# Optimization experiments

Hardware: AMD Instinct MI355X
Metric: run time of the kernel (lower is better)

The kernel has to match this reference:

```python
import jax, jax.numpy as jnp
import numpy as np

Q = 9          # D2Q9
G = 8          # dihedral group of the square
X = YD = 768   # spatial grid
HID = 32       # tau_net hidden width
N_IN = 6       # moments with order <= 2 (indices 0..5, contiguous by construction)
LOWER_TAU = 0.8


def _build_stencil():
    # D2Q9 velocities and weights
    e = np.array([[0, 0], [1, 0], [0, 1], [-1, 0], [0, -1],
                  [1, 1], [-1, 1], [-1, -1], [1, -1]], dtype=np.float64)
    w = np.array([4 / 9] + [1 / 9] * 4 + [1 / 36] * 4, dtype=np.float64)
    # natural moment matrix: rows are monomials ex^px * ey^py, ordered so that
    # moment_order = [0,1,1,2,2,2,3,3,4]  ->  in_indices=[0..5], out_indices=[6,7,8]
    exps = [(0, 0), (1, 0), (0, 1), (2, 0), (1, 1), (0, 2), (2, 1), (1, 2), (2, 2)]
    M = np.stack([e[:, 0] ** px * e[:, 1] ** py for px, py in exps])  # [Q, Q]
    Minv = np.linalg.inv(M)
    # symmetry group of the square: 4 rotations x {id, x-axis reflection}
    rots = [np.array([[np.cos(a), -np.sin(a)], [np.sin(a), np.cos(a)]])
            for a in (0.0, np.pi / 2, np.pi, 3 * np.pi / 2)]
    refl = np.array([[1.0, 0.0], [0.0, -1.0]])
    Rs = rots + [r @ refl for r in rots]
    perms = []
    for R in Rs:
        Re = np.rint(e @ R.T)
        P = np.zeros((Q, Q))
        for i in range(Q):
            j = int(np.where((e == Re[i]).all(axis=1))[0][0])
            P[j, i] = 1.0  # velocity i maps to velocity j under R
        perms.append(P)
    P = np.stack(perms)                                   # [G, Q, Q]
    actions = np.einsum('qp,gpr,rs->gqs', M, P, Minv)      # moment action  M P M^-1
    Pt = P.transpose(0, 2, 1)                              # P^-1 = P^T
    inv_actions = np.einsum('qp,gpr,rs->gqs', M, Pt, Minv)
    return (M.astype(np.float32), Minv.astype(np.float32),
            actions.astype(np.float32), inv_actions.astype(np.float32),
            e.astype(np.float32), w.astype(np.float32))


def setup_inputs() -> dict:
    key = jax.random.key(0)
    kf, k1, k2, k3 = jax.random.split(key, 4)
    M, Minv, actions, inv_actions, e, w = _build_stencil()
    f = jax.random.uniform(kf, (Q, X, YD), dtype=jnp.float32)
    s = 0.1
    return {
        'f': f,
        'M': jnp.asarray(M), 'Minv': jnp.asarray(Minv),
        'actions': jnp.asarray(actions), 'inv_actions': jnp.asarray(inv_actions),
        'e': jnp.asarray(e), 'w': jnp.asarray(w),
        'W1': jax.random.normal(k1, (N_IN, HID), jnp.float32) * s,
        'b1': jnp.zeros((HID,), jnp.float32),
        'W2': jax.random.normal(k2, (HID, HID), jnp.float32) * s,
        'b2': jnp.zeros((HID,), jnp.float32),
        'W3': jax.random.normal(k3, (HID, Q - N_IN), jnp.float32) * s,
        'b3': jnp.zeros((Q - N_IN,), jnp.float32),
    }


def reference(f, M, Minv, actions, inv_actions, e, w, W1, b1, W2, b2, W3, b3):
    # --- moment transform: m = M f, moved to channel-last [X, Y, Q] ---
    m = jnp.einsum('qp,pxy->xyq', M, f)
    # --- equivariant tau net on low-order moments ---
    x_in = m[..., :N_IN]                                   # in_indices = 0..5
    Ainv = inv_actions[:, :N_IN, :N_IN]                    # [G, 6, 6]
    A = actions[:, N_IN:, N_IN:]                           # [G, 3, 3] (out_indices)
    xg = jnp.einsum('gij,xyj->gxyi', Ainv, x_in)           # [G, X, Y, 6]
    h = jax.nn.relu(xg @ W1 + b1)
    h = jax.nn.relu(h @ W2 + b2)
    o = h @ W3 + b3                                        # [G, X, Y, 3]
    out = jnp.einsum('gij,gxyj->xyi', A, o)                # sum over group -> [X, Y, 3]
    tau_hi = 1.5 + jax.nn.elu(out)                         # gt_half: > 0.5
    taus = jnp.full(m.shape, LOWER_TAU, m.dtype).at[..., N_IN:].set(tau_hi)
    # --- equilibrium moments: meq = M feq(rho, u) (quadratic BGK, cs^2=1/3) ---
    rho = m[..., 0:1]                                      # natural moments: m0=rho
    u = m[..., 1:3] / rho                                  # m1,m2 = momentum
    eu = jnp.einsum('qd,xyd->xyq', e, u)
    usq = jnp.sum(u * u, axis=-1, keepdims=True)
    feq = w * rho * (1.0 + 3.0 * eu + 4.5 * eu * eu - 1.5 * usq)
    meq = jnp.einsum('qp,xyp->xyq', M, feq)
    # --- MRT collision + inverse transform ---
    m_post = m - (m - meq) / taus
    return jnp.einsum('pq,xyq->pxy', Minv, m_post)
```

## Files before the change

### kernel.cpp

```cpp
#include <hip/hip_runtime.h>
#include <hip/hip_bf16.h>
#include <math.h>

#define Q 9
#define NPIX (768 * 768)

typedef short bf16x8 __attribute__((ext_vector_type(8)));
typedef float f32x4 __attribute__((ext_vector_type(4)));
typedef int i32x4 __attribute__((ext_vector_type(4)));

#define A1BV 512
#define A3V  1024
#define A2V  1536
#define B3TF 6656

__device__ __forceinline__ unsigned short f2bf(float x) {
    unsigned u = __builtin_bit_cast(unsigned, x);
    unsigned r = u + 0x7FFFu + ((u >> 16) & 1u);
    return (unsigned short)(r >> 16);
}

__device__ __forceinline__ unsigned pk2(float e, float o) {
    __hip_bfloat162 h = __float22bfloat162_rn(make_float2(e, o));
    unsigned u;
    __builtin_memcpy(&u, &h, 4);
    return u;
}

__device__ __forceinline__ bf16x8 mk8(unsigned w0, unsigned w1, unsigned w2, unsigned w3) {
    i32x4 t = {(int)w0, (int)w1, (int)w2, (int)w3};
    return __builtin_bit_cast(bf16x8, t);
}

__global__ void prep_kernel(const float* __restrict__ actions,
                            const float* __restrict__ inv_actions,
                            const float* __restrict__ W1,
                            const float* __restrict__ b1,
                            const float* __restrict__ W2,
                            const float* __restrict__ W3,
                            const float* __restrict__ b3,
                            short* __restrict__ wsb,
                            float* __restrict__ wsf) {
    const int idx = blockIdx.x * 256 + threadIdx.x;
    if (idx < 8192) {
        int j = idx & 7, l = (idx >> 3) & 63, g = (idx >> 9) & 7, half = idx >> 12;
        int m = l & 15, quad = l >> 4, k = quad * 8 + j;
        int feat = 8 * (m >> 2) + (m & 3) + 4 * half;
        float v = 0.f;
        if (k < 6) {
            #pragma unroll
            for (int i = 0; i < 6; i++)
                v += inv_actions[g * 81 + i * 9 + k] * W1[i * 32 + feat];
        } else if (k == 6) v = b1[feat];
        wsb[idx] = (short)f2bf(v);
    } else if (idx < 12288) {
        int t = idx - 8192;
        int j = t & 7, l = (t >> 3) & 63, g = t >> 9;
        int m = l & 15, quad = l >> 4, k = quad * 8 + j;
        float v = 0.f;
        if (m < 3) {
            #pragma unroll
            for (int j3 = 0; j3 < 3; j3++)
                v += W3[k * 3 + j3] * actions[g * 81 + (6 + m) * 9 + (6 + j3)];
        }
        wsb[idx] = (short)f2bf(v);
    } else if (idx < 13312) {
        int t = idx - 12288;
        int j = t & 7, l = (t >> 3) & 63, half = t >> 9;
        int m = l & 15, quad = l >> 4, k = quad * 8 + j;
        int feat = 8 * (m >> 2) + (m & 3) + 4 * half;
        wsb[idx] = (short)f2bf(W2[k * 32 + feat]);
    } else if (idx < 13315) {
        int t = idx - 13312;
        float acc = 0.f;
        for (int g = 0; g < 8; g++)
            #pragma unroll
            for (int j = 0; j < 3; j++)
                acc += actions[g * 81 + (6 + t) * 9 + (6 + j)] * b3[j];
        wsf[B3TF + t] = acc;
    }
}

__global__ __launch_bounds__(256, 4) void lbm_kernel(
    const float* __restrict__ f,
    const float* __restrict__ Minv,
    const float* __restrict__ w,
    const float* __restrict__ b2,
    const short* __restrict__ wsb,
    const float* __restrict__ wsf,
    float* __restrict__ out) {
    __shared__ float oL[4][64][4];

    const int tid = threadIdx.x;
    const int wv = tid >> 6;
    const int l = tid & 63;
    const int quad = l >> 4;
    const int lc = l & 15;
    const int p = blockIdx.x * 256 + tid;

    float fv0 = f[0 * NPIX + p], fv1 = f[1 * NPIX + p], fv2 = f[2 * NPIX + p];
    float fv3 = f[3 * NPIX + p], fv4 = f[4 * NPIX + p], fv5 = f[5 * NPIX + p];
    float fv6 = f[6 * NPIX + p], fv7 = f[7 * NPIX + p], fv8 = f[8 * NPIX + p];
    float sa = fv5 + fv6, sb = fv7 + fv8, sc = fv5 - fv6, sd = fv7 - fv8;
    float sab = sa + sb;
    float m8 = sab, m6 = sa - sb, m4 = sc + sd, m7 = sc - sd;
    float p13 = fv1 + fv3, d13 = fv1 - fv3, p24 = fv2 + fv4, d24 = fv2 - fv4;
    float m0 = fv0 + p13 + p24 + sab;
    float m1 = d13 + m7;
    float m2 = d24 + m6;
    float m3 = p13 + sab;
    float m5 = p24 + sab;

    unsigned mp0 = pk2(m0, m1), mp1 = pk2(m2, m3), mp2 = pk2(m4, m5);
    const unsigned CONE = 0x00003F80u;
    bf16x8 B1[4];
    #pragma unroll
    for (int nb = 0; nb < 4; nb++) {
        int src = ((nb << 4) | lc) << 2;
        unsigned a = (unsigned)__builtin_amdgcn_ds_bpermute(src, (int)mp0);
        unsigned b = (unsigned)__builtin_amdgcn_ds_bpermute(src, (int)mp1);
        unsigned c = (unsigned)__builtin_amdgcn_ds_bpermute(src, (int)mp2);
        B1[nb] = mk8(a, b, c, CONE);
    }

    const bf16x8* wsv = (const bf16x8*)wsb;
    bf16x8 a2a = wsv[A2V + l], a2b = wsv[A2V + 64 + l];
    f32x4 c2iA = *(const f32x4*)(b2 + 8 * quad);
    f32x4 c2iB = *(const f32x4*)(b2 + 8 * quad + 4);
    float b30 = wsf[B3TF + 0], b31 = wsf[B3TF + 1], b32 = wsf[B3TF + 2];
    f32x4 oinit;
    oinit[0] = (quad == 0) ? b30 : 0.f;
    oinit[1] = (quad == 0) ? b31 : 0.f;
    oinit[2] = (quad == 0) ? b32 : 0.f;
    oinit[3] = 0.f;
    f32x4 oacc[4] = {oinit, oinit, oinit, oinit};

    bf16x8 a1a = wsv[l], a1b = wsv[A1BV + l], a3 = wsv[A3V + l];

    #pragma unroll 1
    for (int g = 0; g < 8; g++) {
        const int gn = (g + 1) & 7;
        bf16x8 na1a = wsv[gn * 64 + l];
        bf16x8 na1b = wsv[A1BV + gn * 64 + l];
        bf16x8 na3  = wsv[A3V + gn * 64 + l];
        #pragma unroll
        for (int nb = 0; nb < 4; nb++) {
            f32x4 z = {0.f, 0.f, 0.f, 0.f};
            f32x4 c1a = __builtin_amdgcn_mfma_f32_16x16x32_bf16(a1a, B1[nb], z, 0, 0, 0);
            f32x4 c1b = __builtin_amdgcn_mfma_f32_16x16x32_bf16(a1b, B1[nb], z, 0, 0, 0);
            bf16x8 B2 = mk8(
                pk2(fmaxf(c1a[0], 0.f), fmaxf(c1a[1], 0.f)),
                pk2(fmaxf(c1a[2], 0.f), fmaxf(c1a[3], 0.f)),
                pk2(fmaxf(c1b[0], 0.f), fmaxf(c1b[1], 0.f)),
                pk2(fmaxf(c1b[2], 0.f), fmaxf(c1b[3], 0.f)));
            f32x4 c2a = __builtin_amdgcn_mfma_f32_16x16x32_bf16(a2a, B2, c2iA, 0, 0, 0);
            f32x4 c2b = __builtin_amdgcn_mfma_f32_16x16x32_bf16(a2b, B2, c2iB, 0, 0, 0);
            bf16x8 B3 = mk8(
                pk2(fmaxf(c2a[0], 0.f), fmaxf(c2a[1], 0.f)),
                pk2(fmaxf(c2a[2], 0.f), fmaxf(c2a[3], 0.f)),
                pk2(fmaxf(c2b[0], 0.f), fmaxf(c2b[1], 0.f)),
                pk2(fmaxf(c2b[2], 0.f), fmaxf(c2b[3], 0.f)));
            oacc[nb] = __builtin_amdgcn_mfma_f32_16x16x32_bf16(a3, B3, oacc[nb], 0, 0, 0);
        }
        a1a = na1a; a1b = na1b; a3 = na3;
    }

    if (quad == 0) {
        #pragma unroll
        for (int nb = 0; nb < 4; nb++)
            *(f32x4*)&oL[wv][nb * 16 + lc][0] = oacc[nb];
    }
    f32x4 ov = *(const f32x4*)&oL[wv][l][0];
    float o_[3] = {ov[0], ov[1], ov[2]};

    float tinv[3];
    #pragma unroll
    for (int i = 0; i < 3; i++) {
        float o = o_[i];
        float el = (o > 0.f) ? o : (__expf(o) - 1.f);
        tinv[i] = __builtin_amdgcn_rcpf(1.5f + el);
    }

    float rho = m0;
    float ir = __builtin_amdgcn_rcpf(rho);
    float ux = m1 * ir, uy = m2 * ir;
    float usq = ux * ux + uy * uy;
    float base = 1.f - 1.5f * usq;
    float w0r = w[0] * rho, w1r = w[1] * rho, w5r = w[5] * rho;
    float feq0 = w0r * base;
    float ax = 4.5f * ux * ux + base, bx = 3.f * ux;
    float feq1 = w1r * (ax + bx), feq3 = w1r * (ax - bx);
    float ay = 4.5f * uy * uy + base, by = 3.f * uy;
    float feq2 = w1r * (ay + by), feq4 = w1r * (ay - by);
    float ss = ux + uy, as_ = 4.5f * ss * ss + base, bs = 3.f * ss;
    float feq5 = w5r * (as_ + bs), feq7 = w5r * (as_ - bs);
    float dd = uy - ux, ad = 4.5f * dd * dd + base, bd = 3.f * dd;
    float feq6 = w5r * (ad + bd), feq8 = w5r * (ad - bd);

    float ea = feq5 + feq6, eb = feq7 + feq8, ec = feq5 - feq6, ed = feq7 - feq8;
    float eab = ea + eb;
    float q8 = eab, q6 = ea - eb, q4 = ec + ed, q7 = ec - ed;
    float ep13 = feq1 + feq3, ed13 = feq1 - feq3, ep24 = feq2 + feq4, ed24 = feq2 - feq4;
    float q0 = feq0 + ep13 + ep24 + eab;
    float q1 = ed13 + q7, q2 = ed24 + q6, q3 = ep13 + eab, q5 = ep24 + eab;

    float mp_[9];
    mp_[0] = m0 - (m0 - q0) * 1.25f;
    mp_[1] = m1 - (m1 - q1) * 1.25f;
    mp_[2] = m2 - (m2 - q2) * 1.25f;
    mp_[3] = m3 - (m3 - q3) * 1.25f;
    mp_[4] = m4 - (m4 - q4) * 1.25f;
    mp_[5] = m5 - (m5 - q5) * 1.25f;
    mp_[6] = m6 - (m6 - q6) * tinv[0];
    mp_[7] = m7 - (m7 - q7) * tinv[1];
    mp_[8] = m8 - (m8 - q8) * tinv[2];

    #pragma unroll
    for (int q = 0; q < 9; q++) {
        float acc = Minv[q * 9 + 0] * mp_[0];
        #pragma unroll
        for (int pp = 1; pp < 9; pp++) acc = fmaf(Minv[q * 9 + pp], mp_[pp], acc);
        __builtin_nontemporal_store(acc, &out[q * NPIX + p]);
    }
}

extern "C" void kernel_launch(void* const* d_in, const int* in_sizes, int n_in,
                              void* d_out, int out_size, void* d_ws, size_t ws_size,
                              hipStream_t stream) {
    const float* f           = (const float*)d_in[0];
    const float* Minv        = (const float*)d_in[2];
    const float* actions     = (const float*)d_in[3];
    const float* inv_actions = (const float*)d_in[4];
    const float* w           = (const float*)d_in[6];
    const float* W1          = (const float*)d_in[7];
    const float* b1          = (const float*)d_in[8];
    const float* W2          = (const float*)d_in[9];
    const float* b2          = (const float*)d_in[10];
    const float* W3          = (const float*)d_in[11];
    const float* b3          = (const float*)d_in[12];
    float* outp = (float*)d_out;
    short* wsb = (short*)d_ws;
    float* wsf = (float*)d_ws;

    prep_kernel<<<53, 256, 0, stream>>>(actions, inv_actions, W1, b1, W2, W3, b3, wsb, wsf);
    lbm_kernel<<<NPIX / 256, 256, 0, stream>>>(f, Minv, w, b2, wsb, wsf, outp);
}
```

Before: 135.3 us.

## Rewrite collision epilogue in closed form and reload f to cut register pressure

```diff
diff --git a/kernel.cpp b/kernel.cpp
--- a/kernel.cpp
+++ b/kernel.cpp
@@ -6,6 +6,7 @@
 #define NPIX (768 * 768)
 
 typedef short bf16x8 __attribute__((ext_vector_type(8)));
+typedef short s16x2 __attribute__((ext_vector_type(2)));
 typedef float f32x4 __attribute__((ext_vector_type(4)));
 typedef int i32x4 __attribute__((ext_vector_type(4)));
 
@@ -25,6 +26,13 @@
     unsigned u;
     __builtin_memcpy(&u, &h, 4);
     return u;
+}
+
+__device__ __forceinline__ unsigned relu2(unsigned d) {
+    s16x2 v = __builtin_bit_cast(s16x2, d);
+    const s16x2 z = {0, 0};
+    v = __builtin_elementwise_max(v, z);
+    return __builtin_bit_cast(unsigned, v);
 }
 
 __device__ __forceinline__ bf16x8 mk8(unsigned w0, unsigned w1, unsigned w2, unsigned w3) {
@@ -90,6 +98,8 @@
     const float* __restrict__ wsf,
     float* __restrict__ out) {
     __shared__ float oL[4][64][4];
+    (void)Minv;
+    (void)w;
 
     const int tid = threadIdx.x;
     const int wv = tid >> 6;
@@ -103,11 +113,11 @@
     float fv6 = f[6 * NPIX + p], fv7 = f[7 * NPIX + p], fv8 = f[8 * NPIX + p];
     float sa = fv5 + fv6, sb = fv7 + fv8, sc = fv5 - fv6, sd = fv7 - fv8;
     float sab = sa + sb;
-    float m8 = sab, m6 = sa - sb, m4 = sc + sd, m7 = sc - sd;
+    float m4 = sc + sd;
     float p13 = fv1 + fv3, d13 = fv1 - fv3, p24 = fv2 + fv4, d24 = fv2 - fv4;
     float m0 = fv0 + p13 + p24 + sab;
-    float m1 = d13 + m7;
-    float m2 = d24 + m6;
+    float m1 = d13 + (sc - sd);
+    float m2 = d24 + (sa - sb);
     float m3 = p13 + sab;
     float m5 = p24 + sab;
 
@@ -149,17 +159,17 @@
             f32x4 c1a = __builtin_amdgcn_mfma_f32_16x16x32_bf16(a1a, B1[nb], z, 0, 0, 0);
             f32x4 c1b = __builtin_amdgcn_mfma_f32_16x16x32_bf16(a1b, B1[nb], z, 0, 0, 0);
             bf16x8 B2 = mk8(
-                pk2(fmaxf(c1a[0], 0.f), fmaxf(c1a[1], 0.f)),
-                pk2(fmaxf(c1a[2], 0.f), fmaxf(c1a[3], 0.f)),
-                pk2(fmaxf(c1b[0], 0.f), fmaxf(c1b[1], 0.f)),
-                pk2(fmaxf(c1b[2], 0.f), fmaxf(c1b[3], 0.f)));
+                relu2(pk2(c1a[0], c1a[1])),
+                relu2(pk2(c1a[2], c1a[3])),
+                relu2(pk2(c1b[0], c1b[1])),
+                relu2(pk2(c1b[2], c1b[3])));
             f32x4 c2a = __builtin_amdgcn_mfma_f32_16x16x32_bf16(a2a, B2, c2iA, 0, 0, 0);
             f32x4 c2b = __builtin_amdgcn_mfma_f32_16x16x32_bf16(a2b, B2, c2iB, 0, 0, 0);
             bf16x8 B3 = mk8(
-                pk2(fmaxf(c2a[0], 0.f), fmaxf(c2a[1], 0.f)),
-                pk2(fmaxf(c2a[2], 0.f), fmaxf(c2a[3], 0.f)),
-                pk2(fmaxf(c2b[0], 0.f), fmaxf(c2b[1], 0.f)),
-                pk2(fmaxf(c2b[2], 0.f), fmaxf(c2b[3], 0.f)));
+                relu2(pk2(c2a[0], c2a[1])),
+                relu2(pk2(c2a[2], c2a[3])),
+                relu2(pk2(c2b[0], c2b[1])),
+                relu2(pk2(c2b[2], c2b[3])));
             oacc[nb] = __builtin_amdgcn_mfma_f32_16x16x32_bf16(a3, B3, oacc[nb], 0, 0, 0);
         }
         a1a = na1a; a1b = na1b; a3 = na3;
@@ -171,12 +181,17 @@
             *(f32x4*)&oL[wv][nb * 16 + lc][0] = oacc[nb];
     }
     f32x4 ov = *(const f32x4*)&oL[wv][l][0];
-    float o_[3] = {ov[0], ov[1], ov[2]};
+
+    int p2 = p;
+    asm("" : "+v"(p2));
+    float fr0 = f[0 * NPIX + p2], fr1 = f[1 * NPIX + p2], fr2 = f[2 * NPIX + p2];
+    float fr3 = f[3 * NPIX + p2], fr4 = f[4 * NPIX + p2], fr5 = f[5 * NPIX + p2];
+    float fr6 = f[6 * NPIX + p2], fr7 = f[7 * NPIX + p2], fr8 = f[8 * NPIX + p2];
 
     float tinv[3];
     #pragma unroll
     for (int i = 0; i < 3; i++) {
-        float o = o_[i];
+        float o = ov[i];
         float el = (o > 0.f) ? o : (__expf(o) - 1.f);
         tinv[i] = __builtin_amdgcn_rcpf(1.5f + el);
     }
@@ -186,42 +201,49 @@
     float ux = m1 * ir, uy = m2 * ir;
     float usq = ux * ux + uy * uy;
     float base = 1.f - 1.5f * usq;
-    float w0r = w[0] * rho, w1r = w[1] * rho, w5r = w[5] * rho;
-    float feq0 = w0r * base;
-    float ax = 4.5f * ux * ux + base, bx = 3.f * ux;
+    float w1r = rho * (1.f / 9.f), w5r = rho * (1.f / 36.f);
+    float bx = 3.f * ux, ax = fmaf(4.5f * ux, ux, base);
     float feq1 = w1r * (ax + bx), feq3 = w1r * (ax - bx);
-    float ay = 4.5f * uy * uy + base, by = 3.f * uy;
+    float by = 3.f * uy, ay = fmaf(4.5f * uy, uy, base);
     float feq2 = w1r * (ay + by), feq4 = w1r * (ay - by);
-    float ss = ux + uy, as_ = 4.5f * ss * ss + base, bs = 3.f * ss;
+    float ss = ux + uy, bs = 3.f * ss, as_ = fmaf(4.5f * ss, ss, base);
     float feq5 = w5r * (as_ + bs), feq7 = w5r * (as_ - bs);
-    float dd = uy - ux, ad = 4.5f * dd * dd + base, bd = 3.f * dd;
+    float dd = uy - ux, bd = 3.f * dd, ad = fmaf(4.5f * dd, dd, base);
     float feq6 = w5r * (ad + bd), feq8 = w5r * (ad - bd);
 
-    float ea = feq5 + feq6, eb = feq7 + feq8, ec = feq5 - feq6, ed = feq7 - feq8;
+    float g1 = fr1 - feq1, g2 = fr2 - feq2, g3 = fr3 - feq3, g4 = fr4 - feq4;
+    float g5 = fr5 - feq5, g6 = fr6 - feq6, g7 = fr7 - feq7, g8 = fr8 - feq8;
+    float pa = g1 + g3, pb = g2 + g4;
+    float ea = g5 + g6, eb = g7 + g8, ec = g5 - g6, ed = g7 - g8;
     float eab = ea + eb;
-    float q8 = eab, q6 = ea - eb, q4 = ec + ed, q7 = ec - ed;
-    float ep13 = feq1 + feq3, ed13 = feq1 - feq3, ep24 = feq2 + feq4, ed24 = feq2 - feq4;
-    float q0 = feq0 + ep13 + ep24 + eab;
-    float q1 = ed13 + q7, q2 = ed24 + q6, q3 = ep13 + eab, q5 = ep24 + eab;
-
-    float mp_[9];
-    mp_[0] = m0 - (m0 - q0) * 1.25f;
-    mp_[1] = m1 - (m1 - q1) * 1.25f;
-    mp_[2] = m2 - (m2 - q2) * 1.25f;
-    mp_[3] = m3 - (m3 - q3) * 1.25f;
-    mp_[4] = m4 - (m4 - q4) * 1.25f;
-    mp_[5] = m5 - (m5 - q5) * 1.25f;
-    mp_[6] = m6 - (m6 - q6) * tinv[0];
-    mp_[7] = m7 - (m7 - q7) * tinv[1];
-    mp_[8] = m8 - (m8 - q8) * tinv[2];
-
-    #pragma unroll
-    for (int q = 0; q < 9; q++) {
-        float acc = Minv[q * 9 + 0] * mp_[0];
-        #pragma unroll
-        for (int pp = 1; pp < 9; pp++) acc = fmaf(Minv[q * 9 + pp], mp_[pp], acc);
-        __builtin_nontemporal_store(acc, &out[q * NPIX + p]);
-    }
+    float m3p = pa + eab, m5p = pb + eab, m8p = eab;
+    float m6p = ea - eb, m4p = ec + ed, m7p = ec - ed;
+
+    float d3 = 1.25f * m3p, h3 = 0.625f * m3p;
+    float d5 = 1.25f * m5p, h5 = 0.625f * m5p;
+    float k4 = 0.3125f * m4p;
+    float h6 = (0.5f * tinv[0]) * m6p, k6 = 0.5f * h6;
+    float h7 = (0.5f * tinv[1]) * m7p, k7 = 0.5f * h7;
+    float d8 = tinv[2] * m8p, h8 = 0.5f * d8, k8 = 0.5f * h8;
+
+    float c0 = d8 - d3 - d5;
+    float c1 = h3 - h7 - h8;
+    float c2 = h5 - h6 - h8;
+    float c3 = h3 + h7 - h8;
+    float c4 = h5 + h6 - h8;
+    float sA = k4 + k7, sB = k6 + k8, sC = k4 + k8;
+    float sD = k6 + k7, sE = k7 + k8, sF = k4 + k6;
+    float c5 = sA + sB, c6 = sB - sA, c7 = sC - sD, c8 = sE - sF;
+
+    __builtin_nontemporal_store(fr0 - c0, &out[0 * NPIX + p]);
+    __builtin_nontemporal_store(fr1 - c1, &out[1 * NPIX + p]);
+    __builtin_nontemporal_store(fr2 - c2, &out[2 * NPIX + p]);
+    __builtin_nontemporal_store(fr3 - c3, &out[3 * NPIX + p]);
+    __builtin_nontemporal_store(fr4 - c4, &out[4 * NPIX + p]);
+    __builtin_nontemporal_store(fr5 - c5, &out[5 * NPIX + p]);
+    __builtin_nontemporal_store(fr6 - c6, &out[6 * NPIX + p]);
+    __builtin_nontemporal_store(fr7 - c7, &out[7 * NPIX + p]);
+    __builtin_nontemporal_store(fr8 - c8, &out[8 * NPIX + p]);
 }
 
 extern "C" void kernel_launch(void* const* d_in, const int* in_sizes, int n_in,
```

Measured after the change: 121.1 us. 1.12x faster.
